# Kernel optimization log

Measured on AMD Instinct MI355X. Metric: run time of the kernel, lower is better.

Reference implementation:

```python
import jax, jax.numpy as jnp
import numpy as np

N, E = 50000, 800000
IN, HID, OUT = 128, 128, 64
H, ED = 4, 3
D = HID // H  # per-head dim = 32


def _w(key, shape):
    fan_in = shape[-1]
    return jax.random.normal(key, shape, dtype=jnp.float32) / np.sqrt(fan_in)


def setup_inputs() -> dict:
    key = jax.random.key(0)
    ks = jax.random.split(key, 32)
    inp = {
        "x": jax.random.normal(ks[0], (N, IN), dtype=jnp.float32),
        "edge_index": jax.random.randint(ks[1], (2, E), 0, N, dtype=jnp.int32),
        "edge_attr": jax.random.normal(ks[2], (E, ED), dtype=jnp.float32),
        # layer 1 TransformerConv (bias=False)
        "Wq1": _w(ks[3], (HID, IN)), "Wk1": _w(ks[4], (HID, IN)),
        "Wv1": _w(ks[5], (HID, IN)), "We1": _w(ks[6], (HID, ED)),
        "Ws1": _w(ks[7], (HID, IN)),
        # layer 1 MLP [HID,HID,HID]
        "M1a": _w(ks[8], (HID, HID)), "b1a": jnp.zeros((HID,), jnp.float32),
        "M1b": _w(ks[9], (HID, HID)), "b1b": jnp.zeros((HID,), jnp.float32),
        # layer 2 TransformerConv
        "Wq2": _w(ks[10], (HID, HID)), "Wk2": _w(ks[11], (HID, HID)),
        "Wv2": _w(ks[12], (HID, HID)), "We2": _w(ks[13], (HID, ED)),
        "Ws2": _w(ks[14], (HID, HID)),
        # layer 2 MLP
        "M2a": _w(ks[15], (HID, HID)), "b2a": jnp.zeros((HID,), jnp.float32),
        "M2b": _w(ks[16], (HID, HID)), "b2b": jnp.zeros((HID,), jnp.float32),
        # final MLP [HID,HID,OUT], plain_last=False
        "Wf1": _w(ks[17], (HID, HID)), "bf1": jnp.zeros((HID,), jnp.float32),
        "Wf2": _w(ks[18], (OUT, HID)), "bf2": jnp.zeros((OUT,), jnp.float32),
    }
    return inp


def _gelu(x):
    return jax.nn.gelu(x, approximate=True)


def _transformer_conv(x, src, dst, edge_attr, Wq, Wk, Wv, We, Ws, n_nodes):
    # PyG TransformerConv: x_j = x[src] (message source), x_i = x[dst] (target)
    q = (x @ Wq.T).reshape(n_nodes, H, D)
    e = (edge_attr @ We.T).reshape(-1, H, D)              # [E,H,D]
    k = (x @ Wk.T).reshape(n_nodes, H, D)[src] + e        # [E,H,D]
    v = (x @ Wv.T).reshape(n_nodes, H, D)[src] + e        # [E,H,D]
    alpha = jnp.einsum("ehd,ehd->eh", q[dst], k) / jnp.float32(np.sqrt(D))
    # segment softmax over incoming edges of each target node
    m = jax.ops.segment_max(alpha, dst, num_segments=n_nodes)  # [N,H]
    m = jnp.where(jnp.isfinite(m), m, 0.0)
    p = jnp.exp(alpha - m[dst])
    s = jax.ops.segment_sum(p, dst, num_segments=n_nodes)      # [N,H]
    a = p / jnp.maximum(s[dst], 1e-16)                         # [E,H]
    out = jax.ops.segment_sum(a[:, :, None] * v, dst, num_segments=n_nodes)
    out = out.reshape(n_nodes, H * D)
    # root_weight=True (default): skip connection through lin_skip (no bias)
    return out + x @ Ws.T


def _mlp2(x, Wa, ba, Wb, bb):
    # PyG MLP with plain_last=False: act after every linear, norm=None
    h = _gelu(x @ Wa.T + ba)
    return _gelu(h @ Wb.T + bb)


def reference(x, edge_index, edge_attr,
              Wq1, Wk1, Wv1, We1, Ws1, M1a, b1a, M1b, b1b,
              Wq2, Wk2, Wv2, We2, Ws2, M2a, b2a, M2b, b2b,
              Wf1, bf1, Wf2, bf2):
    n_nodes = x.shape[0]
    src, dst = edge_index[0], edge_index[1]
    h = _transformer_conv(x, src, dst, edge_attr, Wq1, Wk1, Wv1, We1, Ws1, n_nodes)
    h = h + _mlp2(h, M1a, b1a, M1b, b1b)
    h = _transformer_conv(h, src, dst, edge_attr, Wq2, Wk2, Wv2, We2, Ws2, n_nodes)
    h = h + _mlp2(h, M2a, b2a, M2b, b2b)
    return _mlp2(h, Wf1, bf1, Wf2, bf2)
```

## Files before the change

kernel.cpp:

```cpp
#include <hip/hip_runtime.h>
#include <hip/hip_bf16.h>
#include <math.h>

#define NN 50000
#define NE 800000
#define NPAD 50048
#define NB_SCAN 196

typedef unsigned short u16;
typedef unsigned int u32;
typedef __attribute__((ext_vector_type(8))) short short8;
typedef __attribute__((ext_vector_type(4))) float float4v;

__device__ __forceinline__ float us2f(u16 u) { return __uint_as_float(((unsigned)u) << 16); }
__device__ __forceinline__ float blo(u32 u) { return __uint_as_float(u << 16); }
__device__ __forceinline__ float bhi(u32 u) { return __uint_as_float(u & 0xffff0000u); }
__device__ __forceinline__ u16 f2us(float f) {
    unsigned x = __float_as_uint(f);
    return (u16)((x + 0x7FFFu + ((x >> 16) & 1u)) >> 16);
}
__device__ __forceinline__ float gelu_f(float x) {
    float p = x * x;
    float t = x * fmaf(p, 0.0713548162726f, 1.5957691216057308f);
    float e = __expf(-t);
    return x * __builtin_amdgcn_rcpf(1.0f + e);
}
__device__ __forceinline__ void lds_fence() {
    asm volatile("s_waitcnt lgkmcnt(0)" ::: "memory");
}

__device__ __forceinline__ float4v mfma4p(const u16* __restrict__ WP, int tile, int l,
                                          short8 a0, short8 a1, short8 a2, short8 a3) {
    const short8* wp = (const short8*)WP + (size_t)tile * 256 + l;
    short8 b0 = wp[0], b1 = wp[64], b2 = wp[128], b3 = wp[192];
    float4v acc = {0.f, 0.f, 0.f, 0.f};
    acc = __builtin_amdgcn_mfma_f32_16x16x32_bf16(a0, b0, acc, 0, 0, 0);
    acc = __builtin_amdgcn_mfma_f32_16x16x32_bf16(a1, b1, acc, 0, 0, 0);
    acc = __builtin_amdgcn_mfma_f32_16x16x32_bf16(a2, b2, acc, 0, 0, 0);
    acc = __builtin_amdgcn_mfma_f32_16x16x32_bf16(a3, b3, acc, 0, 0, 0);
    return acc;
}


__global__ void k_hist(const int* __restrict__ dstv, int* __restrict__ deg) {
    int e = blockIdx.x * blockDim.x + threadIdx.x;
    if (e < NE) atomicAdd(&deg[dstv[e]], 1);
}

__global__ __launch_bounds__(256) void k_scan1(const int* __restrict__ deg,
                                               int* __restrict__ rowstart,
                                               int* __restrict__ bsum) {
    __shared__ int wtot[4];
    int i = blockIdx.x * 256 + threadIdx.x;
    int lane = threadIdx.x & 63, w = threadIdx.x >> 6;
    int v = (i < NN) ? deg[i] : 0;
    int incl = v;
#pragma unroll
    for (int d = 1; d < 64; d <<= 1) {
        int tv = __shfl_up(incl, d);
        if (lane >= d) incl += tv;
    }
    if (lane == 63) wtot[w] = incl;
    __syncthreads();
    if (threadIdx.x == 0) {
        int s = 0;
#pragma unroll
        for (int j = 0; j < 4; ++j) { int t = wtot[j]; wtot[j] = s; s += t; }
        bsum[blockIdx.x] = s;
    }
    __syncthreads();
    if (i < NN) rowstart[i] = incl - v + wtot[w];
}

__global__ __launch_bounds__(256) void k_scan2(int* __restrict__ bsum) {
    __shared__ int wtot[4];
    int t = threadIdx.x;
    int lane = t & 63, w = t >> 6;
    int v = (t < NB_SCAN) ? bsum[t] : 0;
    int incl = v;
#pragma unroll
    for (int d = 1; d < 64; d <<= 1) {
        int tv = __shfl_up(incl, d);
        if (lane >= d) incl += tv;
    }
    if (lane == 63) wtot[w] = incl;
    __syncthreads();
    if (t == 0) {
        int s = 0;
#pragma unroll
        for (int j = 0; j < 4; ++j) { int tt = wtot[j]; wtot[j] = s; s += tt; }
    }
    __syncthreads();
    if (t < NB_SCAN) bsum[t] = incl - v + wtot[w];
}

__global__ void k_scan3(const int* __restrict__ bsum, int* __restrict__ rowstart,
                        int* __restrict__ cursor) {
    int i = blockIdx.x * 256 + threadIdx.x;
    if (i < NN) {
        int v = rowstart[i] + bsum[blockIdx.x];
        rowstart[i] = v;
        cursor[i] = v;
    }
    if (i == 0) rowstart[NN] = NE;
}

__global__ void k_scatter(const int* __restrict__ srcv, const int* __restrict__ dstv,
                          const float* __restrict__ eattr, int* __restrict__ cursor,
                          int4* __restrict__ rec) {
    int e = blockIdx.x * blockDim.x + threadIdx.x;
    if (e >= NE) return;
    int dst = dstv[e];
    int pos = atomicAdd(&cursor[dst], 1);
    int4 r;
    r.x = srcv[e];
    r.y = __float_as_int(eattr[e * 3 + 0]);
    r.z = __float_as_int(eattr[e * 3 + 1]);
    r.w = __float_as_int(eattr[e * 3 + 2]);
    rec[pos] = r;
}


struct CvtEnt { const float* s; u16* d; int n; };
struct CvtTab { CvtEnt e[14]; };
__global__ void k_cvt_w(CvtTab tab) {
    CvtEnt E = tab.e[blockIdx.x >> 3];
    int chunk = blockIdx.x & 7;
    int per = E.n >> 3;
    int lo = chunk * per, hi = lo + per;
    for (int o = lo + threadIdx.x; o < hi; o += blockDim.x) {
        int tile = o >> 11;
        int q = (o >> 9) & 3;
        int l = (o >> 3) & 63;
        int j = o & 7;
        int row = tile * 16 + (l & 15);
        int col = q * 32 + (l >> 4) * 8 + j;
        E.d[o] = f2us(E.s[row * 128 + col]);
    }
}

__global__ void k_prep_we(const float* __restrict__ We1, const float* __restrict__ We2,
                          float4* __restrict__ WeP1, float4* __restrict__ WeP2) {
    int t = threadIdx.x;
    if (t < 128) {
        WeP1[t] = make_float4(We1[t * 3], We1[t * 3 + 1], We1[t * 3 + 2], 0.f);
    } else {
        int c = t - 128;
        WeP2[c] = make_float4(We2[c * 3], We2[c * 3 + 1], We2[c * 3 + 2], 0.f);
    }
}


__device__ __forceinline__ void stage_plain(u16* buf, int kb, int m, int tt, float4v acc) {
#pragma unroll
    for (int r = 0; r < 4; ++r) buf[(kb * 4 + r) * 136 + tt * 16 + m] = f2us(acc[r]);
}
__device__ __forceinline__ void store128(const u16* buf, u16* dst, int r0w, int coff, int l) {
#pragma unroll
    for (int it = 0; it < 4; ++it) {
        int j = it * 64 + l;
        int row = j >> 4, col = (j & 15) * 8;
        *(uint4*)(dst + (size_t)(r0w + row) * 512 + coff + col) = *(const uint4*)&buf[row * 136 + col];
    }
}
__device__ __forceinline__ void read_frags(const u16* buf, int m, int kb,
                                           short8& f0, short8& f1, short8& f2, short8& f3) {
    const u16* p = buf + m * 136 + kb * 8;
    f0 = *(const short8*)(p);
    f1 = *(const short8*)(p + 32);
    f2 = *(const short8*)(p + 64);
    f3 = *(const short8*)(p + 96);
}

__device__ __forceinline__ void compute_g(const u16* buf, const float4* __restrict__ WeP,
                                          float4* __restrict__ G, int r0w, int m, int kb) {
    const u16* qr = buf + m * 136 + kb * 32;
    short8 qv0 = *(const short8*)(qr);
    short8 qv1 = *(const short8*)(qr + 8);
    short8 qv2 = *(const short8*)(qr + 16);
    short8 qv3 = *(const short8*)(qr + 24);
    const float4* wp = WeP + kb * 32;
    float g0 = 0.f, g1 = 0.f, g2 = 0.f;
    const short8* qs[4] = {&qv0, &qv1, &qv2, &qv3};
#pragma unroll
    for (int b = 0; b < 4; ++b) {
        const u16* qq = (const u16*)qs[b];
#pragma unroll
        for (int d = 0; d < 8; ++d) {
            float qvf = us2f(qq[d]);
            float4 wv = wp[b * 8 + d];
            g0 = fmaf(qvf, wv.x, g0);
            g1 = fmaf(qvf, wv.y, g1);
            g2 = fmaf(qvf, wv.z, g2);
        }
    }
    G[(size_t)(r0w + m) * 4 + kb] = make_float4(g0, g1, g2, 0.f);
}



__global__ __launch_bounds__(64, 4) void k_qkvs1(const float* __restrict__ Ain,
                                                 const u16* __restrict__ W,
                                                 const float4* __restrict__ WeP,
                                                 float4* __restrict__ G,
                                                 u16* __restrict__ QKVS) {
    __shared__ u16 my[16 * 136];
    int l = threadIdx.x;
    int m = l & 15, kb = l >> 4;
    int r0w = blockIdx.x * 16;

    short8 a0, a1, a2, a3;
    {
        const float* ap = Ain + (size_t)(r0w + m) * 128;
        bool ok = (r0w + m) < NN;
        short8* dsts[4] = {&a0, &a1, &a2, &a3};
#pragma unroll
        for (int i = 0; i < 4; ++i) {
            short8 r;
            if (ok) {
                const float* p = ap + (kb + i * 4) * 8;
                float4 f0 = *(const float4*)p;
                float4 f1 = *(const float4*)(p + 4);
                r[0]=(short)f2us(f0.x); r[1]=(short)f2us(f0.y); r[2]=(short)f2us(f0.z); r[3]=(short)f2us(f0.w);
                r[4]=(short)f2us(f1.x); r[5]=(short)f2us(f1.y); r[6]=(short)f2us(f1.z); r[7]=(short)f2us(f1.w);
            } else {
#pragma unroll
                for (int j = 0; j < 8; ++j) r[j] = 0;
            }
            *dsts[i] = r;
        }
    }

#pragma unroll
    for (int tt = 0; tt < 8; ++tt) stage_plain(my, kb, m, tt, mfma4p(W, tt, l, a0, a1, a2, a3));
    lds_fence();
    store128(my, QKVS, r0w, 0, l);
    compute_g(my, WeP, G, r0w, m, kb);
    lds_fence();
#pragma unroll
    for (int tt = 0; tt < 4; ++tt) {
        float4v acc = mfma4p(W, 8 + tt, l, a0, a1, a2, a3);
        int c = tt * 32 + 8 * (m >> 2) + (m & 3);
#pragma unroll
        for (int r = 0; r < 4; ++r) my[(kb * 4 + r) * 136 + c] = f2us(acc[r]);
    }
#pragma unroll
    for (int tt = 0; tt < 4; ++tt) {
        float4v acc = mfma4p(W, 16 + tt, l, a0, a1, a2, a3);
        int c = tt * 32 + 8 * (m >> 2) + (m & 3) + 4;
#pragma unroll
        for (int r = 0; r < 4; ++r) my[(kb * 4 + r) * 136 + c] = f2us(acc[r]);
    }
    lds_fence();
    store128(my, QKVS, r0w, 128, l);
    lds_fence();
#pragma unroll
    for (int tt = 0; tt < 4; ++tt) {
        float4v acc = mfma4p(W, 12 + tt, l, a0, a1, a2, a3);
        int c = tt * 32 + 8 * (m >> 2) + (m & 3);
#pragma unroll
        for (int r = 0; r < 4; ++r) my[(kb * 4 + r) * 136 + c] = f2us(acc[r]);
    }
#pragma unroll
    for (int tt = 0; tt < 4; ++tt) {
        float4v acc = mfma4p(W, 20 + tt, l, a0, a1, a2, a3);
        int c = tt * 32 + 8 * (m >> 2) + (m & 3) + 4;
#pragma unroll
        for (int r = 0; r < 4; ++r) my[(kb * 4 + r) * 136 + c] = f2us(acc[r]);
    }
    lds_fence();
    store128(my, QKVS, r0w, 256, l);
    lds_fence();
#pragma unroll
    for (int tt = 0; tt < 8; ++tt) stage_plain(my, kb, m, tt, mfma4p(W, 24 + tt, l, a0, a1, a2, a3));
    lds_fence();
    store128(my, QKVS, r0w, 384, l);
}


__global__ __launch_bounds__(64, 4) void k_mlp_qkvs(const u16* __restrict__ Ain,
                                                    const u16* __restrict__ Wm,
                                                    const float* __restrict__ bias1,
                                                    const float* __restrict__ bias2,
                                                    const u16* __restrict__ Wq,
                                                    const float4* __restrict__ WeP,
                                                    float4* __restrict__ G,
                                                    u16* __restrict__ QKVS) {
    __shared__ u16 sh[16 * 136];
    __shared__ u16 t1[16 * 136];
    int l = threadIdx.x;
    int m = l & 15, kb = l >> 4;
    int r0w = blockIdx.x * 16;

    const short8* arow = (const short8*)(Ain + (size_t)(r0w + m) * 128);
    short8 a0 = arow[kb], a1 = arow[kb + 4], a2 = arow[kb + 8], a3 = arow[kb + 12];
    {
        u16* p = sh + m * 136 + kb * 8;
        *(short8*)(p) = a0;
        *(short8*)(p + 32) = a1;
        *(short8*)(p + 64) = a2;
        *(short8*)(p + 96) = a3;
    }
#pragma unroll
    for (int tt = 0; tt < 8; ++tt) {
        float4v acc = mfma4p(Wm, tt, l, a0, a1, a2, a3);
        float bv = bias1[tt * 16 + m];
#pragma unroll
        for (int r = 0; r < 4; ++r)
            t1[(kb * 4 + r) * 136 + tt * 16 + m] = f2us(gelu_f(acc[r] + bv));
    }
    lds_fence();
    short8 c0, c1, c2, c3;
    read_frags(t1, m, kb, c0, c1, c2, c3);
#pragma unroll
    for (int tt = 0; tt < 8; ++tt) {
        float4v acc = mfma4p(Wm + 16384, tt, l, c0, c1, c2, c3);
        float bv = bias2[tt * 16 + m];
#pragma unroll
        for (int r = 0; r < 4; ++r) {
            int idx = (kb * 4 + r) * 136 + tt * 16 + m;
            sh[idx] = f2us(gelu_f(acc[r] + bv) + us2f(sh[idx]));
        }
    }
    lds_fence();
    short8 h0, h1, h2, h3;
    read_frags(sh, m, kb, h0, h1, h2, h3);

#pragma unroll
    for (int tt = 0; tt < 8; ++tt) stage_plain(t1, kb, m, tt, mfma4p(Wq, tt, l, h0, h1, h2, h3));
    lds_fence();
    store128(t1, QKVS, r0w, 0, l);
    compute_g(t1, WeP, G, r0w, m, kb);
    lds_fence();
#pragma unroll
    for (int tt = 0; tt < 4; ++tt) {
        float4v acc = mfma4p(Wq, 8 + tt, l, h0, h1, h2, h3);
        int c = tt * 32 + 8 * (m >> 2) + (m & 3);
#pragma unroll
        for (int r = 0; r < 4; ++r) t1[(kb * 4 + r) * 136 + c] = f2us(acc[r]);
    }
#pragma unroll
    for (int tt = 0; tt < 4; ++tt) {
        float4v acc = mfma4p(Wq, 16 + tt, l, h0, h1, h2, h3);
        int c = tt * 32 + 8 * (m >> 2) + (m & 3) + 4;
#pragma unroll
        for (int r = 0; r < 4; ++r) t1[(kb * 4 + r) * 136 + c] = f2us(acc[r]);
    }
    lds_fence();
    store128(t1, QKVS, r0w, 128, l);
    lds_fence();
#pragma unroll
    for (int tt = 0; tt < 4; ++tt) {
        float4v acc = mfma4p(Wq, 12 + tt, l, h0, h1, h2, h3);
        int c = tt * 32 + 8 * (m >> 2) + (m & 3);
#pragma unroll
        for (int r = 0; r < 4; ++r) t1[(kb * 4 + r) * 136 + c] = f2us(acc[r]);
    }
#pragma unroll
    for (int tt = 0; tt < 4; ++tt) {
        float4v acc = mfma4p(Wq, 20 + tt, l, h0, h1, h2, h3);
        int c = tt * 32 + 8 * (m >> 2) + (m & 3) + 4;
#pragma unroll
        for (int r = 0; r < 4; ++r) t1[(kb * 4 + r) * 136 + c] = f2us(acc[r]);
    }
    lds_fence();
    store128(t1, QKVS, r0w, 256, l);
    lds_fence();
#pragma unroll
    for (int tt = 0; tt < 8; ++tt) stage_plain(t1, kb, m, tt, mfma4p(Wq, 24 + tt, l, h0, h1, h2, h3));
    lds_fence();
    store128(t1, QKVS, r0w, 384, l);
}


__global__ __launch_bounds__(64, 4) void k_mlp_final(const u16* __restrict__ Ain,
                                                     const u16* __restrict__ Wm,
                                                     const float* __restrict__ bias1,
                                                     const float* __restrict__ bias2,
                                                     const u16* __restrict__ Wf,
                                                     const float* __restrict__ bf1,
                                                     const float* __restrict__ bf2,
                                                     float* __restrict__ outp) {
    __shared__ u16 sh[16 * 136];
    __shared__ u16 t1[16 * 136];
    int l = threadIdx.x;
    int m = l & 15, kb = l >> 4;
    int r0w = blockIdx.x * 16;

    const short8* arow = (const short8*)(Ain + (size_t)(r0w + m) * 128);
    short8 a0 = arow[kb], a1 = arow[kb + 4], a2 = arow[kb + 8], a3 = arow[kb + 12];
    {
        u16* p = sh + m * 136 + kb * 8;
        *(short8*)(p) = a0;
        *(short8*)(p + 32) = a1;
        *(short8*)(p + 64) = a2;
        *(short8*)(p + 96) = a3;
    }
#pragma unroll
    for (int tt = 0; tt < 8; ++tt) {
        float4v acc = mfma4p(Wm, tt, l, a0, a1, a2, a3);
        float bv = bias1[tt * 16 + m];
#pragma unroll
        for (int r = 0; r < 4; ++r)
            t1[(kb * 4 + r) * 136 + tt * 16 + m] = f2us(gelu_f(acc[r] + bv));
    }
    lds_fence();
    short8 c0, c1, c2, c3;
    read_frags(t1, m, kb, c0, c1, c2, c3);
#pragma unroll
    for (int tt = 0; tt < 8; ++tt) {
        float4v acc = mfma4p(Wm + 16384, tt, l, c0, c1, c2, c3);
        float bv = bias2[tt * 16 + m];
#pragma unroll
        for (int r = 0; r < 4; ++r) {
            int idx = (kb * 4 + r) * 136 + tt * 16 + m;
            sh[idx] = f2us(gelu_f(acc[r] + bv) + us2f(sh[idx]));
        }
    }
    lds_fence();
    short8 h0, h1, h2, h3;
    read_frags(sh, m, kb, h0, h1, h2, h3);
#pragma unroll
    for (int tt = 0; tt < 8; ++tt) {
        float4v acc = mfma4p(Wf, tt, l, h0, h1, h2, h3);
        float bv = bf1[tt * 16 + m];
#pragma unroll
        for (int r = 0; r < 4; ++r)
            t1[(kb * 4 + r) * 136 + tt * 16 + m] = f2us(gelu_f(acc[r] + bv));
    }
    lds_fence();
    short8 f0, f1, f2, f3;
    read_frags(t1, m, kb, f0, f1, f2, f3);
    lds_fence();
#pragma unroll
    for (int tt = 0; tt < 4; ++tt) {
        float4v acc = mfma4p(Wf + 16384, tt, l, f0, f1, f2, f3);
        float bv = bf2[tt * 16 + m];
#pragma unroll
        for (int r = 0; r < 4; ++r)
            t1[(kb * 4 + r) * 136 + tt * 16 + m] = f2us(gelu_f(acc[r] + bv));
    }
    lds_fence();
#pragma unroll
    for (int it = 0; it < 2; ++it) {
        int j = it * 64 + l;
        int row = j >> 3, col = (j & 7) * 8;
        int grow = r0w + row;
        if (grow < NN) {
            uint4 pk = *(const uint4*)&t1[row * 136 + col];
            const u16* pv = (const u16*)&pk;
            float* po = outp + (size_t)grow * 64 + col;
            float4 o0 = {us2f(pv[0]), us2f(pv[1]), us2f(pv[2]), us2f(pv[3])};
            float4 o1 = {us2f(pv[4]), us2f(pv[5]), us2f(pv[6]), us2f(pv[7])};
            *(float4*)po = o0;
            *(float4*)(po + 4) = o1;
        }
    }
}


__global__ __launch_bounds__(256) void k_conv(const int* __restrict__ rowstart,
                                              const int4* __restrict__ rec,
                                              const u16* __restrict__ qkvs,
                                              const float4* __restrict__ WeP,
                                              const float4* __restrict__ G,
                                              u16* __restrict__ out) {
    int n = blockIdx.x * 4 + (threadIdx.x >> 6);
    int l = threadIdx.x & 63;
    int quarter = l >> 4;
    int li = l & 15;
    int c0 = li * 8;
    const u16* qrow = qkvs + (size_t)n * 512;
    uint4 qu = *(const uint4*)(qrow + c0);
    const float SC = 0.17677669529663687f;
    float q0 = blo(qu.x) * SC, q1 = bhi(qu.x) * SC, q2 = blo(qu.y) * SC, q3 = bhi(qu.y) * SC;
    float q4 = blo(qu.z) * SC, q5 = bhi(qu.z) * SC, q6 = blo(qu.w) * SC, q7 = bhi(qu.w) * SC;
    float4 gg = G[(size_t)n * 4 + (li >> 2)];
    float g0 = gg.x * SC, g1 = gg.y * SC, g2 = gg.z * SC;

    int e0 = rowstart[n], e1 = rowstart[n + 1];
    int deg = e1 - e0;
    float ss = 0.f, S0 = 0.f, S1 = 0.f, S2 = 0.f;
    float o0 = 0.f, o1 = 0.f, o2 = 0.f, o3 = 0.f, o4 = 0.f, o5 = 0.f, o6 = 0.f, o7 = 0.f;

    if (deg > 0) {
        int iters = (deg + 3) >> 2;
        int eb = e0 + quarter;
        int elast = e1 - 1;
        int4 r0 = rec[min(eb, elast)];
        int4 r1 = rec[min(eb + 4, elast)];
        const u16* kvB = qkvs + 128 + (size_t)li * 16;
        uint4 kA = *(const uint4*)(kvB + (size_t)r0.x * 512);
        uint4 kB = *(const uint4*)(kvB + (size_t)r0.x * 512 + 8);
        for (int i = 0; i < iters; ++i) {
            int4 r2 = rec[min(eb + 4 * (i + 2), elast)];
            const u16* kp = kvB + (size_t)r1.x * 512;
            uint4 nA = *(const uint4*)(kp);
            uint4 nB = *(const uint4*)(kp + 8);
            float part = q0 * blo(kA.x) + q1 * bhi(kA.x) + q2 * blo(kA.y) + q3 * bhi(kA.y)
                       + q4 * blo(kB.x) + q5 * bhi(kB.x) + q6 * blo(kB.y) + q7 * bhi(kB.y);
            part += __shfl_xor(part, 1);
            part += __shfl_xor(part, 2);
            float ea0 = __int_as_float(r0.y), ea1 = __int_as_float(r0.z), ea2 = __int_as_float(r0.w);
            float alpha = fmaf(ea2, g2, fmaf(ea1, g1, fmaf(ea0, g0, part)));
            float p = __expf(fminf(alpha, 80.f));
            p = (eb + 4 * i < e1) ? p : 0.f;
            o0 = fmaf(p, blo(kA.z), o0);
            o1 = fmaf(p, bhi(kA.z), o1);
            o2 = fmaf(p, blo(kA.w), o2);
            o3 = fmaf(p, bhi(kA.w), o3);
            o4 = fmaf(p, blo(kB.z), o4);
            o5 = fmaf(p, bhi(kB.z), o5);
            o6 = fmaf(p, blo(kB.w), o6);
            o7 = fmaf(p, bhi(kB.w), o7);
            ss += p;
            S0 = fmaf(p, ea0, S0);
            S1 = fmaf(p, ea1, S1);
            S2 = fmaf(p, ea2, S2);
            r0 = r1; r1 = r2; kA = nA; kB = nB;
        }
    }
    o0 += __shfl_xor(o0, 16); o1 += __shfl_xor(o1, 16); o2 += __shfl_xor(o2, 16); o3 += __shfl_xor(o3, 16);
    o4 += __shfl_xor(o4, 16); o5 += __shfl_xor(o5, 16); o6 += __shfl_xor(o6, 16); o7 += __shfl_xor(o7, 16);
    ss += __shfl_xor(ss, 16); S0 += __shfl_xor(S0, 16); S1 += __shfl_xor(S1, 16); S2 += __shfl_xor(S2, 16);
    o0 += __shfl_xor(o0, 32); o1 += __shfl_xor(o1, 32); o2 += __shfl_xor(o2, 32); o3 += __shfl_xor(o3, 32);
    o4 += __shfl_xor(o4, 32); o5 += __shfl_xor(o5, 32); o6 += __shfl_xor(o6, 32); o7 += __shfl_xor(o7, 32);
    ss += __shfl_xor(ss, 32); S0 += __shfl_xor(S0, 32); S1 += __shfl_xor(S1, 32); S2 += __shfl_xor(S2, 32);

    if (quarter == 0) {
        float inv = __builtin_amdgcn_rcpf(fmaxf(ss, 1e-16f));
        float4 w0 = WeP[c0 + 0], w1 = WeP[c0 + 1], w2 = WeP[c0 + 2], w3 = WeP[c0 + 3];
        float4 w4 = WeP[c0 + 4], w5 = WeP[c0 + 5], w6 = WeP[c0 + 6], w7 = WeP[c0 + 7];
        o0 += w0.x * S0 + w0.y * S1 + w0.z * S2;
        o1 += w1.x * S0 + w1.y * S1 + w1.z * S2;
        o2 += w2.x * S0 + w2.y * S1 + w2.z * S2;
        o3 += w3.x * S0 + w3.y * S1 + w3.z * S2;
        o4 += w4.x * S0 + w4.y * S1 + w4.z * S2;
        o5 += w5.x * S0 + w5.y * S1 + w5.z * S2;
        o6 += w6.x * S0 + w6.y * S1 + w6.z * S2;
        o7 += w7.x * S0 + w7.y * S1 + w7.z * S2;
        uint4 su = *(const uint4*)(qrow + 384 + c0);
        float r0v = fmaf(o0, inv, blo(su.x));
        float r1v = fmaf(o1, inv, bhi(su.x));
        float r2v = fmaf(o2, inv, blo(su.y));
        float r3v = fmaf(o3, inv, bhi(su.y));
        float r4v = fmaf(o4, inv, blo(su.z));
        float r5v = fmaf(o5, inv, bhi(su.z));
        float r6v = fmaf(o6, inv, blo(su.w));
        float r7v = fmaf(o7, inv, bhi(su.w));
        uint4 ou;
        ou.x = (u32)f2us(r0v) | ((u32)f2us(r1v) << 16);
        ou.y = (u32)f2us(r2v) | ((u32)f2us(r3v) << 16);
        ou.z = (u32)f2us(r4v) | ((u32)f2us(r5v) << 16);
        ou.w = (u32)f2us(r6v) | ((u32)f2us(r7v) << 16);
        *(uint4*)(out + (size_t)n * 128 + c0) = ou;
    }
}


extern "C" void kernel_launch(void* const* d_in, const int* in_sizes, int n_in,
                              void* d_out, int out_size, void* d_ws, size_t ws_size,
                              hipStream_t stream) {
    const float* x = (const float*)d_in[0];
    const int* ei = (const int*)d_in[1];
    const float* eattr = (const float*)d_in[2];
    const float* Wq1 = (const float*)d_in[3];
    const float* Wk1 = (const float*)d_in[4];
    const float* Wv1 = (const float*)d_in[5];
    const float* We1 = (const float*)d_in[6];
    const float* Ws1 = (const float*)d_in[7];
    const float* M1a = (const float*)d_in[8];
    const float* b1a = (const float*)d_in[9];
    const float* M1b = (const float*)d_in[10];
    const float* b1b = (const float*)d_in[11];
    const float* Wq2 = (const float*)d_in[12];
    const float* Wk2 = (const float*)d_in[13];
    const float* Wv2 = (const float*)d_in[14];
    const float* We2 = (const float*)d_in[15];
    const float* Ws2 = (const float*)d_in[16];
    const float* M2a = (const float*)d_in[17];
    const float* b2a = (const float*)d_in[18];
    const float* M2b = (const float*)d_in[19];
    const float* b2b = (const float*)d_in[20];
    const float* Wf1 = (const float*)d_in[21];
    const float* bf1 = (const float*)d_in[22];
    const float* Wf2 = (const float*)d_in[23];
    const float* bf2 = (const float*)d_in[24];

    char* ws = (char*)d_ws;
    size_t off = 0;
    auto alloc = [&](size_t bytes) -> void* {
        void* p = ws + off;
        off = (off + bytes + 255) & ~(size_t)255;
        return p;
    };
    int* deg = (int*)alloc((size_t)NN * 4);
    int* rowstart = (int*)alloc((size_t)(NN + 1) * 4);
    int* cursor = (int*)alloc((size_t)NN * 4);
    int* bsum = (int*)alloc((size_t)NB_SCAN * 4);
    int4* rec = (int4*)alloc((size_t)NE * 16);
    u16* QKVS = (u16*)alloc((size_t)NPAD * 512 * 2);
    u16* Ha = (u16*)alloc((size_t)NPAD * 128 * 2);
    float4* G = (float4*)alloc((size_t)NPAD * 4 * 16);
    float4* WeP1 = (float4*)alloc(128 * 16);
    float4* WeP2 = (float4*)alloc(128 * 16);
    u16* WB[14];
    const int wsz[14] = {16384, 16384, 16384, 16384, 16384, 16384, 16384,
                         16384, 16384, 16384, 16384, 16384, 16384, 8192};
    for (int i = 0; i < 14; ++i) WB[i] = (u16*)alloc((size_t)wsz[i] * 2);

    const int* srcv = ei;
    const int* dstv = ei + NE;

    hipMemsetAsync(deg, 0, (size_t)NN * 4, stream);
    k_hist<<<(NE + 255) / 256, 256, 0, stream>>>(dstv, deg);
    k_scan1<<<NB_SCAN, 256, 0, stream>>>(deg, rowstart, bsum);
    k_scan2<<<1, 256, 0, stream>>>(bsum);
    k_scan3<<<NB_SCAN, 256, 0, stream>>>(bsum, rowstart, cursor);
    k_scatter<<<(NE + 255) / 256, 256, 0, stream>>>(srcv, dstv, eattr, cursor, rec);

    CvtTab tab;
    const float* wsrc[14] = {Wq1, Wk1, Wv1, Ws1, Wq2, Wk2, Wv2, Ws2,
                             M1a, M1b, M2a, M2b, Wf1, Wf2};
    for (int i = 0; i < 14; ++i) { tab.e[i].s = wsrc[i]; tab.e[i].d = WB[i]; tab.e[i].n = wsz[i]; }
    k_cvt_w<<<112, 256, 0, stream>>>(tab);
    k_prep_we<<<1, 256, 0, stream>>>(We1, We2, WeP1, WeP2);

    dim3 gg(NPAD / 16);
    dim3 gconv(NN / 4);

    k_qkvs1<<<gg, 64, 0, stream>>>(x, WB[0], WeP1, G, QKVS);
    k_conv<<<gconv, 256, 0, stream>>>(rowstart, rec, QKVS, WeP1, G, Ha);
    k_mlp_qkvs<<<gg, 64, 0, stream>>>(Ha, WB[8], b1a, b1b, WB[4], WeP2, G, QKVS);
    k_conv<<<gconv, 256, 0, stream>>>(rowstart, rec, QKVS, WeP2, G, Ha);
    k_mlp_final<<<gg, 64, 0, stream>>>(Ha, WB[10], b2a, b2b, WB[12], bf1, bf2, (float*)d_out);
}
```

Before: 412.1 us.

## Split fused node GEMM kernels into persistent register-resident-weight GEMM stages

Replaces the fused per-16-row QKVS and MLP kernels with a generic persistent templated GEMM kernel. Each block loads its weight slice into registers once, then loops over row tiles, so weights are no longer re-read from global memory for every tile. Output columns are split across blockIdx.y sections. The fused MLP chains become separate launches that round-trip intermediates (Tb, Hb) through global memory. This trades extra launches and intermediate traffic for weight reuse and more parallelism, at the cost of heavy register pressure from holding the weights.

```diff
diff --git a/kernel.cpp b/kernel.cpp
--- a/kernel.cpp
+++ b/kernel.cpp
@@ -5,6 +5,7 @@
 #define NN 50000
 #define NE 800000
 #define NPAD 50048
+#define NTILES 3125
 #define NB_SCAN 196
 
 typedef unsigned short u16;
@@ -29,15 +30,13 @@
     asm volatile("s_waitcnt lgkmcnt(0)" ::: "memory");
 }
 
-__device__ __forceinline__ float4v mfma4p(const u16* __restrict__ WP, int tile, int l,
-                                          short8 a0, short8 a1, short8 a2, short8 a3) {
-    const short8* wp = (const short8*)WP + (size_t)tile * 256 + l;
-    short8 b0 = wp[0], b1 = wp[64], b2 = wp[128], b3 = wp[192];
+__device__ __forceinline__ float4v mfma4b(short8 a0, short8 a1, short8 a2, short8 a3,
+                                          const short8* B) {
     float4v acc = {0.f, 0.f, 0.f, 0.f};
-    acc = __builtin_amdgcn_mfma_f32_16x16x32_bf16(a0, b0, acc, 0, 0, 0);
-    acc = __builtin_amdgcn_mfma_f32_16x16x32_bf16(a1, b1, acc, 0, 0, 0);
-    acc = __builtin_amdgcn_mfma_f32_16x16x32_bf16(a2, b2, acc, 0, 0, 0);
-    acc = __builtin_amdgcn_mfma_f32_16x16x32_bf16(a3, b3, acc, 0, 0, 0);
+    acc = __builtin_amdgcn_mfma_f32_16x16x32_bf16(a0, B[0], acc, 0, 0, 0);
+    acc = __builtin_amdgcn_mfma_f32_16x16x32_bf16(a1, B[1], acc, 0, 0, 0);
+    acc = __builtin_amdgcn_mfma_f32_16x16x32_bf16(a2, B[2], acc, 0, 0, 0);
+    acc = __builtin_amdgcn_mfma_f32_16x16x32_bf16(a3, B[3], acc, 0, 0, 0);
     return acc;
 }
 
@@ -151,10 +150,6 @@
 }
 
 
-__device__ __forceinline__ void stage_plain(u16* buf, int kb, int m, int tt, float4v acc) {
-#pragma unroll
-    for (int r = 0; r < 4; ++r) buf[(kb * 4 + r) * 136 + tt * 16 + m] = f2us(acc[r]);
-}
 __device__ __forceinline__ void store128(const u16* buf, u16* dst, int r0w, int coff, int l) {
 #pragma unroll
     for (int it = 0; it < 4; ++it) {
@@ -163,28 +158,16 @@
         *(uint4*)(dst + (size_t)(r0w + row) * 512 + coff + col) = *(const uint4*)&buf[row * 136 + col];
     }
 }
-__device__ __forceinline__ void read_frags(const u16* buf, int m, int kb,
-                                           short8& f0, short8& f1, short8& f2, short8& f3) {
-    const u16* p = buf + m * 136 + kb * 8;
-    f0 = *(const short8*)(p);
-    f1 = *(const short8*)(p + 32);
-    f2 = *(const short8*)(p + 64);
-    f3 = *(const short8*)(p + 96);
-}
 
 __device__ __forceinline__ void compute_g(const u16* buf, const float4* __restrict__ WeP,
                                           float4* __restrict__ G, int r0w, int m, int kb) {
     const u16* qr = buf + m * 136 + kb * 32;
-    short8 qv0 = *(const short8*)(qr);
-    short8 qv1 = *(const short8*)(qr + 8);
-    short8 qv2 = *(const short8*)(qr + 16);
-    short8 qv3 = *(const short8*)(qr + 24);
     const float4* wp = WeP + kb * 32;
     float g0 = 0.f, g1 = 0.f, g2 = 0.f;
-    const short8* qs[4] = {&qv0, &qv1, &qv2, &qv3};
 #pragma unroll
     for (int b = 0; b < 4; ++b) {
-        const u16* qq = (const u16*)qs[b];
+        short8 qv = *(const short8*)(qr + b * 8);
+        const u16* qq = (const u16*)&qv;
 #pragma unroll
         for (int d = 0; d < 8; ++d) {
             float qvf = us2f(qq[d]);
@@ -197,264 +180,148 @@
     G[(size_t)(r0w + m) * 4 + kb] = make_float4(g0, g1, g2, 0.f);
 }
 
-
-
-__global__ __launch_bounds__(64, 4) void k_qkvs1(const float* __restrict__ Ain,
+__device__ __forceinline__ void load_a32(const float* __restrict__ A, int row, int kb,
+                                         short8& a0, short8& a1, short8& a2, short8& a3) {
+    const float* ap = A + (size_t)row * 128;
+    short8* dsts[4] = {&a0, &a1, &a2, &a3};
+#pragma unroll
+    for (int i = 0; i < 4; ++i) {
+        const float* p = ap + (kb + i * 4) * 8;
+        float4 f0 = *(const float4*)p;
+        float4 f1 = *(const float4*)(p + 4);
+        short8 r;
+        r[0]=(short)f2us(f0.x); r[1]=(short)f2us(f0.y); r[2]=(short)f2us(f0.z); r[3]=(short)f2us(f0.w);
+        r[4]=(short)f2us(f1.x); r[5]=(short)f2us(f1.y); r[6]=(short)f2us(f1.z); r[7]=(short)f2us(f1.w);
+        *dsts[i] = r;
+    }
+}
+__device__ __forceinline__ void load_a16(const u16* __restrict__ A, int row, int kb,
+                                         short8& a0, short8& a1, short8& a2, short8& a3) {
+    const short8* arow = (const short8*)(A + (size_t)row * 128);
+    a0 = arow[kb]; a1 = arow[kb + 4]; a2 = arow[kb + 8]; a3 = arow[kb + 12];
+}
+
+template <bool A32, int NT, bool GCOMP, bool GELU_, bool RES, bool F32OUT>
+__global__ __launch_bounds__(64, 2) void k_gs(const void* __restrict__ Ain,
+                                              const u16* __restrict__ W,
+                                              const float* __restrict__ bias,
+                                              const u16* __restrict__ res,
+                                              void* __restrict__ outp,
+                                              int ostride, int ocol,
+                                              int sec_tile_mul, int sec_coff_mul,
+                                              const float4* __restrict__ WeP,
+                                              float4* __restrict__ G) {
+    __shared__ u16 my[16 * 136];
+    int l = threadIdx.x;
+    int m = l & 15, kb = l >> 4;
+    const u16* Wsec = W + (size_t)blockIdx.y * sec_tile_mul * 2048;
+    int coff = ocol + blockIdx.y * sec_coff_mul;
+    bool do_g = GCOMP && (blockIdx.y == 0);
+
+    short8 B[NT][4];
+#pragma unroll
+    for (int t = 0; t < NT; ++t) {
+        const short8* wp = (const short8*)Wsec + (size_t)t * 256 + l;
+        B[t][0] = wp[0]; B[t][1] = wp[64]; B[t][2] = wp[128]; B[t][3] = wp[192];
+    }
+    float bv[NT];
+    if (GELU_) {
+#pragma unroll
+        for (int t = 0; t < NT; ++t) bv[t] = bias[t * 16 + m];
+    }
+
+    for (int rt = blockIdx.x; rt < NTILES; rt += gridDim.x) {
+        int r0w = rt * 16;
+        short8 a0, a1, a2, a3;
+        if (A32) load_a32((const float*)Ain, r0w + m, kb, a0, a1, a2, a3);
+        else     load_a16((const u16*)Ain, r0w + m, kb, a0, a1, a2, a3);
+#pragma unroll
+        for (int tt = 0; tt < NT; ++tt) {
+            float4v acc = mfma4b(a0, a1, a2, a3, B[tt]);
+#pragma unroll
+            for (int r = 0; r < 4; ++r) {
+                float v = acc[r];
+                if (GELU_) v = gelu_f(v + bv[tt]);
+                my[(kb * 4 + r) * 136 + tt * 16 + m] = f2us(v);
+            }
+        }
+        lds_fence();
+        if (do_g) compute_g(my, WeP, G, r0w, m, kb);
+        if (F32OUT) {
+#pragma unroll
+            for (int it = 0; it < 2; ++it) {
+                int j = it * 64 + l;
+                int row = j >> 3, col = (j & 7) * 8;
+                uint4 pk = *(const uint4*)&my[row * 136 + col];
+                const u16* pv = (const u16*)&pk;
+                float* po = (float*)outp + (size_t)(r0w + row) * 64 + col;
+                float4 o0 = {us2f(pv[0]), us2f(pv[1]), us2f(pv[2]), us2f(pv[3])};
+                float4 o1 = {us2f(pv[4]), us2f(pv[5]), us2f(pv[6]), us2f(pv[7])};
+                *(float4*)po = o0;
+                *(float4*)(po + 4) = o1;
+            }
+        } else {
+#pragma unroll
+            for (int it = 0; it < 4; ++it) {
+                int j = it * 64 + l;
+                int row = j >> 4, col = (j & 15) * 8;
+                uint4 pk = *(const uint4*)&my[row * 136 + col];
+                if (RES) {
+                    uint4 rk = *(const uint4*)(res + (size_t)(r0w + row) * 128 + col);
+                    u16* po = (u16*)&pk;
+                    const u16* pr = (const u16*)&rk;
+#pragma unroll
+                    for (int j2 = 0; j2 < 8; ++j2) po[j2] = f2us(us2f(po[j2]) + us2f(pr[j2]));
+                }
+                *(uint4*)((u16*)outp + (size_t)(r0w + row) * ostride + coff + col) = pk;
+            }
+        }
+        lds_fence();
+    }
+}
+
+template <bool A32>
+__global__ __launch_bounds__(64, 2) void k_gs_kv(const void* __restrict__ Ain,
                                                  const u16* __restrict__ W,
-                                                 const float4* __restrict__ WeP,
-                                                 float4* __restrict__ G,
                                                  u16* __restrict__ QKVS) {
     __shared__ u16 my[16 * 136];
     int l = threadIdx.x;
     int m = l & 15, kb = l >> 4;
-    int r0w = blockIdx.x * 16;
-
-    short8 a0, a1, a2, a3;
-    {
-        const float* ap = Ain + (size_t)(r0w + m) * 128;
-        bool ok = (r0w + m) < NN;
-        short8* dsts[4] = {&a0, &a1, &a2, &a3};
-#pragma unroll
-        for (int i = 0; i < 4; ++i) {
-            short8 r;
-            if (ok) {
-                const float* p = ap + (kb + i * 4) * 8;
-                float4 f0 = *(const float4*)p;
-                float4 f1 = *(const float4*)(p + 4);
-                r[0]=(short)f2us(f0.x); r[1]=(short)f2us(f0.y); r[2]=(short)f2us(f0.z); r[3]=(short)f2us(f0.w);
-                r[4]=(short)f2us(f1.x); r[5]=(short)f2us(f1.y); r[6]=(short)f2us(f1.z); r[7]=(short)f2us(f1.w);
-            } else {
-#pragma unroll
-                for (int j = 0; j < 8; ++j) r[j] = 0;
-            }
-            *dsts[i] = r;
+    int kbase = 8 + 4 * blockIdx.y;
+    int vbase = 16 + 4 * blockIdx.y;
+    int coff = 128 + 128 * blockIdx.y;
+
+    short8 Bk[4][4], Bv[4][4];
+#pragma unroll
+    for (int t = 0; t < 4; ++t) {
+        const short8* wk = (const short8*)W + (size_t)(kbase + t) * 256 + l;
+        Bk[t][0] = wk[0]; Bk[t][1] = wk[64]; Bk[t][2] = wk[128]; Bk[t][3] = wk[192];
+        const short8* wv = (const short8*)W + (size_t)(vbase + t) * 256 + l;
+        Bv[t][0] = wv[0]; Bv[t][1] = wv[64]; Bv[t][2] = wv[128]; Bv[t][3] = wv[192];
+    }
+
+    for (int rt = blockIdx.x; rt < NTILES; rt += gridDim.x) {
+        int r0w = rt * 16;
+        short8 a0, a1, a2, a3;
+        if (A32) load_a32((const float*)Ain, r0w + m, kb, a0, a1, a2, a3);
+        else     load_a16((const u16*)Ain, r0w + m, kb, a0, a1, a2, a3);
+#pragma unroll
+        for (int tt = 0; tt < 4; ++tt) {
+            float4v acc = mfma4b(a0, a1, a2, a3, Bk[tt]);
+            int c = tt * 32 + 8 * (m >> 2) + (m & 3);
+#pragma unroll
+            for (int r = 0; r < 4; ++r) my[(kb * 4 + r) * 136 + c] = f2us(acc[r]);
         }
-    }
-
-#pragma unroll
-    for (int tt = 0; tt < 8; ++tt) stage_plain(my, kb, m, tt, mfma4p(W, tt, l, a0, a1, a2, a3));
-    lds_fence();
-    store128(my, QKVS, r0w, 0, l);
-    compute_g(my, WeP, G, r0w, m, kb);
-    lds_fence();
-#pragma unroll
-    for (int tt = 0; tt < 4; ++tt) {
-        float4v acc = mfma4p(W, 8 + tt, l, a0, a1, a2, a3);
-        int c = tt * 32 + 8 * (m >> 2) + (m & 3);
-#pragma unroll
-        for (int r = 0; r < 4; ++r) my[(kb * 4 + r) * 136 + c] = f2us(acc[r]);
-    }
-#pragma unroll
-    for (int tt = 0; tt < 4; ++tt) {
-        float4v acc = mfma4p(W, 16 + tt, l, a0, a1, a2, a3);
-        int c = tt * 32 + 8 * (m >> 2) + (m & 3) + 4;
-#pragma unroll
-        for (int r = 0; r < 4; ++r) my[(kb * 4 + r) * 136 + c] = f2us(acc[r]);
-    }
-    lds_fence();
-    store128(my, QKVS, r0w, 128, l);
-    lds_fence();
-#pragma unroll
-    for (int tt = 0; tt < 4; ++tt) {
-        float4v acc = mfma4p(W, 12 + tt, l, a0, a1, a2, a3);
-        int c = tt * 32 + 8 * (m >> 2) + (m & 3);
-#pragma unroll
-        for (int r = 0; r < 4; ++r) my[(kb * 4 + r) * 136 + c] = f2us(acc[r]);
-    }
-#pragma unroll
-    for (int tt = 0; tt < 4; ++tt) {
-        float4v acc = mfma4p(W, 20 + tt, l, a0, a1, a2, a3);
-        int c = tt * 32 + 8 * (m >> 2) + (m & 3) + 4;
-#pragma unroll
-        for (int r = 0; r < 4; ++r) my[(kb * 4 + r) * 136 + c] = f2us(acc[r]);
-    }
-    lds_fence();
-    store128(my, QKVS, r0w, 256, l);
-    lds_fence();
-#pragma unroll
-    for (int tt = 0; tt < 8; ++tt) stage_plain(my, kb, m, tt, mfma4p(W, 24 + tt, l, a0, a1, a2, a3));
-    lds_fence();
-    store128(my, QKVS, r0w, 384, l);
-}
-
-
-__global__ __launch_bounds__(64, 4) void k_mlp_qkvs(const u16* __restrict__ Ain,
-                                                    const u16* __restrict__ Wm,
-                                                    const float* __restrict__ bias1,
-                                                    const float* __restrict__ bias2,
-                                                    const u16* __restrict__ Wq,
-                                                    const float4* __restrict__ WeP,
-                                                    float4* __restrict__ G,
-                                                    u16* __restrict__ QKVS) {
-    __shared__ u16 sh[16 * 136];
-    __shared__ u16 t1[16 * 136];
-    int l = threadIdx.x;
-    int m = l & 15, kb = l >> 4;
-    int r0w = blockIdx.x * 16;
-
-    const short8* arow = (const short8*)(Ain + (size_t)(r0w + m) * 128);
-    short8 a0 = arow[kb], a1 = arow[kb + 4], a2 = arow[kb + 8], a3 = arow[kb + 12];
-    {
-        u16* p = sh + m * 136 + kb * 8;
-        *(short8*)(p) = a0;
-        *(short8*)(p + 32) = a1;
-        *(short8*)(p + 64) = a2;
-        *(short8*)(p + 96) = a3;
-    }
-#pragma unroll
-    for (int tt = 0; tt < 8; ++tt) {
-        float4v acc = mfma4p(Wm, tt, l, a0, a1, a2, a3);
-        float bv = bias1[tt * 16 + m];
-#pragma unroll
-        for (int r = 0; r < 4; ++r)
-            t1[(kb * 4 + r) * 136 + tt * 16 + m] = f2us(gelu_f(acc[r] + bv));
-    }
-    lds_fence();
-    short8 c0, c1, c2, c3;
-    read_frags(t1, m, kb, c0, c1, c2, c3);
-#pragma unroll
-    for (int tt = 0; tt < 8; ++tt) {
-        float4v acc = mfma4p(Wm + 16384, tt, l, c0, c1, c2, c3);
-        float bv = bias2[tt * 16 + m];
-#pragma unroll
-        for (int r = 0; r < 4; ++r) {
-            int idx = (kb * 4 + r) * 136 + tt * 16 + m;
-            sh[idx] = f2us(gelu_f(acc[r] + bv) + us2f(sh[idx]));
+#pragma unroll
+        for (int tt = 0; tt < 4; ++tt) {
+            float4v acc = mfma4b(a0, a1, a2, a3, Bv[tt]);
+            int c = tt * 32 + 8 * (m >> 2) + (m & 3) + 4;
+#pragma unroll
+            for (int r = 0; r < 4; ++r) my[(kb * 4 + r) * 136 + c] = f2us(acc[r]);
         }
-    }
-    lds_fence();
-    short8 h0, h1, h2, h3;
-    read_frags(sh, m, kb, h0, h1, h2, h3);
-
-#pragma unroll
-    for (int tt = 0; tt < 8; ++tt) stage_plain(t1, kb, m, tt, mfma4p(Wq, tt, l, h0, h1, h2, h3));
-    lds_fence();
-    store128(t1, QKVS, r0w, 0, l);
-    compute_g(t1, WeP, G, r0w, m, kb);
-    lds_fence();
-#pragma unroll
-    for (int tt = 0; tt < 4; ++tt) {
-        float4v acc = mfma4p(Wq, 8 + tt, l, h0, h1, h2, h3);
-        int c = tt * 32 + 8 * (m >> 2) + (m & 3);
-#pragma unroll
-        for (int r = 0; r < 4; ++r) t1[(kb * 4 + r) * 136 + c] = f2us(acc[r]);
-    }
-#pragma unroll
-    for (int tt = 0; tt < 4; ++tt) {
-        float4v acc = mfma4p(Wq, 16 + tt, l, h0, h1, h2, h3);
-        int c = tt * 32 + 8 * (m >> 2) + (m & 3) + 4;
-#pragma unroll
-        for (int r = 0; r < 4; ++r) t1[(kb * 4 + r) * 136 + c] = f2us(acc[r]);
-    }
-    lds_fence();
-    store128(t1, QKVS, r0w, 128, l);
-    lds_fence();
-#pragma unroll
-    for (int tt = 0; tt < 4; ++tt) {
-        float4v acc = mfma4p(Wq, 12 + tt, l, h0, h1, h2, h3);
-        int c = tt * 32 + 8 * (m >> 2) + (m & 3);
-#pragma unroll
-        for (int r = 0; r < 4; ++r) t1[(kb * 4 + r) * 136 + c] = f2us(acc[r]);
-    }
-#pragma unroll
-    for (int tt = 0; tt < 4; ++tt) {
-        float4v acc = mfma4p(Wq, 20 + tt, l, h0, h1, h2, h3);
-        int c = tt * 32 + 8 * (m >> 2) + (m & 3) + 4;
-#pragma unroll
-        for (int r = 0; r < 4; ++r) t1[(kb * 4 + r) * 136 + c] = f2us(acc[r]);
-    }
-    lds_fence();
-    store128(t1, QKVS, r0w, 256, l);
-    lds_fence();
-#pragma unroll
-    for (int tt = 0; tt < 8; ++tt) stage_plain(t1, kb, m, tt, mfma4p(Wq, 24 + tt, l, h0, h1, h2, h3));
-    lds_fence();
-    store128(t1, QKVS, r0w, 384, l);
-}
-
-
-__global__ __launch_bounds__(64, 4) void k_mlp_final(const u16* __restrict__ Ain,
-                                                     const u16* __restrict__ Wm,
-                                                     const float* __restrict__ bias1,
-                                                     const float* __restrict__ bias2,
-                                                     const u16* __restrict__ Wf,
-                                                     const float* __restrict__ bf1,
-                                                     const float* __restrict__ bf2,
-                                                     float* __restrict__ outp) {
-    __shared__ u16 sh[16 * 136];
-    __shared__ u16 t1[16 * 136];
-    int l = threadIdx.x;
-    int m = l & 15, kb = l >> 4;
-    int r0w = blockIdx.x * 16;
-
-    const short8* arow = (const short8*)(Ain + (size_t)(r0w + m) * 128);
-    short8 a0 = arow[kb], a1 = arow[kb + 4], a2 = arow[kb + 8], a3 = arow[kb + 12];
-    {
-        u16* p = sh + m * 136 + kb * 8;
-        *(short8*)(p) = a0;
-        *(short8*)(p + 32) = a1;
-        *(short8*)(p + 64) = a2;
-        *(short8*)(p + 96) = a3;
-    }
-#pragma unroll
-    for (int tt = 0; tt < 8; ++tt) {
-        float4v acc = mfma4p(Wm, tt, l, a0, a1, a2, a3);
-        float bv = bias1[tt * 16 + m];
-#pragma unroll
-        for (int r = 0; r < 4; ++r)
-            t1[(kb * 4 + r) * 136 + tt * 16 + m] = f2us(gelu_f(acc[r] + bv));
-    }
-    lds_fence();
-    short8 c0, c1, c2, c3;
-    read_frags(t1, m, kb, c0, c1, c2, c3);
-#pragma unroll
-    for (int tt = 0; tt < 8; ++tt) {
-        float4v acc = mfma4p(Wm + 16384, tt, l, c0, c1, c2, c3);
-        float bv = bias2[tt * 16 + m];
-#pragma unroll
-        for (int r = 0; r < 4; ++r) {
-            int idx = (kb * 4 + r) * 136 + tt * 16 + m;
-            sh[idx] = f2us(gelu_f(acc[r] + bv) + us2f(sh[idx]));
-        }
-    }
-    lds_fence();
-    short8 h0, h1, h2, h3;
-    read_frags(sh, m, kb, h0, h1, h2, h3);
-#pragma unroll
-    for (int tt = 0; tt < 8; ++tt) {
-        float4v acc = mfma4p(Wf, tt, l, h0, h1, h2, h3);
-        float bv = bf1[tt * 16 + m];
-#pragma unroll
-        for (int r = 0; r < 4; ++r)
-            t1[(kb * 4 + r) * 136 + tt * 16 + m] = f2us(gelu_f(acc[r] + bv));
-    }
-    lds_fence();
-    short8 f0, f1, f2, f3;
-    read_frags(t1, m, kb, f0, f1, f2, f3);
-    lds_fence();
-#pragma unroll
-    for (int tt = 0; tt < 4; ++tt) {
-        float4v acc = mfma4p(Wf + 16384, tt, l, f0, f1, f2, f3);
-        float bv = bf2[tt * 16 + m];
-#pragma unroll
-        for (int r = 0; r < 4; ++r)
-            t1[(kb * 4 + r) * 136 + tt * 16 + m] = f2us(gelu_f(acc[r] + bv));
-    }
-    lds_fence();
-#pragma unroll
-    for (int it = 0; it < 2; ++it) {
-        int j = it * 64 + l;
-        int row = j >> 3, col = (j & 7) * 8;
-        int grow = r0w + row;
-        if (grow < NN) {
-            uint4 pk = *(const uint4*)&t1[row * 136 + col];
-            const u16* pv = (const u16*)&pk;
-            float* po = outp + (size_t)grow * 64 + col;
-            float4 o0 = {us2f(pv[0]), us2f(pv[1]), us2f(pv[2]), us2f(pv[3])};
-            float4 o1 = {us2f(pv[4]), us2f(pv[5]), us2f(pv[6]), us2f(pv[7])};
-            *(float4*)po = o0;
-            *(float4*)(po + 4) = o1;
-        }
+        lds_fence();
+        store128(my, QKVS, r0w, coff, l);
+        lds_fence();
     }
 }
 
@@ -601,6 +468,8 @@
     int4* rec = (int4*)alloc((size_t)NE * 16);
     u16* QKVS = (u16*)alloc((size_t)NPAD * 512 * 2);
     u16* Ha = (u16*)alloc((size_t)NPAD * 128 * 2);
+    u16* Hb = (u16*)alloc((size_t)NPAD * 128 * 2);
+    u16* Tb = (u16*)alloc((size_t)NPAD * 128 * 2);
     float4* G = (float4*)alloc((size_t)NPAD * 4 * 16);
     float4* WeP1 = (float4*)alloc(128 * 16);
     float4* WeP2 = (float4*)alloc(128 * 16);
@@ -626,12 +495,31 @@
     k_cvt_w<<<112, 256, 0, stream>>>(tab);
     k_prep_we<<<1, 256, 0, stream>>>(We1, We2, WeP1, WeP2);
 
-    dim3 gg(NPAD / 16);
+    dim3 gqs(2048, 2);
+    dim3 gkv(2048, 2);
+    dim3 gm(2048);
     dim3 gconv(NN / 4);
 
-    k_qkvs1<<<gg, 64, 0, stream>>>(x, WB[0], WeP1, G, QKVS);
+    k_gs<true, 8, true, false, false, false><<<gqs, 64, 0, stream>>>(
+        x, WB[0], nullptr, nullptr, QKVS, 512, 0, 24, 384, WeP1, G);
+    k_gs_kv<true><<<gkv, 64, 0, stream>>>(x, WB[0], QKVS);
     k_conv<<<gconv, 256, 0, stream>>>(rowstart, rec, QKVS, WeP1, G, Ha);
-    k_mlp_qkvs<<<gg, 64, 0, stream>>>(Ha, WB[8], b1a, b1b, WB[4], WeP2, G, QKVS);
+    k_gs<false, 8, false, true, false, false><<<gm, 64, 0, stream>>>(
+        Ha, WB[8], b1a, nullptr, Tb, 128, 0, 0, 0, nullptr, nullptr);
+    k_gs<false, 8, false, true, true, false><<<gm, 64, 0, stream>>>(
+        Tb, WB[9], b1b, Ha, Hb, 128, 0, 0, 0, nullptr, nullptr);
+
+    k_gs<false, 8, true, false, false, false><<<gqs, 64, 0, stream>>>(
+        Hb, WB[4], nullptr, nullptr, QKVS, 512, 0, 24, 384, WeP2, G);
+    k_gs_kv<false><<<gkv, 64, 0, stream>>>(Hb, WB[4], QKVS);
     k_conv<<<gconv, 256, 0, stream>>>(rowstart, rec, QKVS, WeP2, G, Ha);
-    k_mlp_final<<<gg, 64, 0, stream>>>(Ha, WB[10], b2a, b2b, WB[12], bf1, bf2, (float*)d_out);
-}
+    k_gs<false, 8, false, true, false, false><<<gm, 64, 0, stream>>>(
+        Ha, WB[10], b2a, nullptr, Tb, 128, 0, 0, 0, nullptr, nullptr);
+    k_gs<false, 8, false, true, true, false><<<gm, 64, 0, stream>>>(
+        Tb, WB[11], b2b, Ha, Hb, 128, 0, 0, 0, nullptr, nullptr);
+
+    k_gs<false, 8, false, true, false, false><<<gm, 64, 0, stream>>>(
+        Hb, WB[12], bf1, nullptr, Tb, 128, 0, 0, 0, nullptr, nullptr);
+    k_gs<false, 4, false, true, false, true><<<gm, 64, 0, stream>>>(
+        Tb, WB[13], bf2, nullptr, d_out, 64, 0, 0, 0, nullptr, nullptr);
+}
```

Result: slower. 459.2 us (+11.4%).
